# Performance work log

Measured on AMD Instinct MI355X. Metric: run time of the kernel, lower is better.

Reference implementation:

```python
import jax, jax.numpy as jnp
import numpy as np

N_POINTS = 131072
N_SEG = 16
C = 256
BN_EPS = 1e-5


def setup_inputs() -> dict:
    key = jax.random.key(0)
    ks = jax.random.split(key, 6)
    x = jax.random.normal(ks[0], (N_POINTS, C), jnp.float32)
    # Ragged segment end-offsets (cumulative counts), strictly increasing, last == N_POINTS.
    rng = np.random.default_rng(0)
    base = N_POINTS // N_SEG
    counts = base + rng.integers(-base // 32, base // 32, N_SEG)
    counts[-1] += N_POINTS - counts.sum()
    o = jnp.asarray(np.cumsum(counts), jnp.int32)
    s1 = 1.0 / np.sqrt(2 * C)  # linear1: Linear(2C -> C)
    s2 = 1.0 / np.sqrt(C)      # linear2: Linear(C -> C)
    W1 = jax.random.uniform(ks[1], (2 * C, C), jnp.float32, -s1, s1)
    b1 = jax.random.uniform(ks[2], (C,), jnp.float32, -s1, s1)
    W2 = jax.random.uniform(ks[3], (C, C), jnp.float32, -s2, s2)
    b2 = jax.random.uniform(ks[4], (C,), jnp.float32, -s2, s2)
    gamma = jnp.ones((C,), jnp.float32)
    beta = jnp.zeros((C,), jnp.float32)
    return {"x": x, "o": o, "W1": W1, "b1": b1, "W2": W2, "b2": b2,
            "gamma": gamma, "beta": beta}


def reference(x, o, W1, b1, W2, b2, gamma, beta):
    n, c = x.shape
    s = o.shape[0]
    # segment id per point from cumulative end-offsets
    seg_id = jnp.searchsorted(o, jnp.arange(n), side="right")  # [N]
    counts = jnp.concatenate([o[:1], o[1:] - o[:-1]])          # [S]
    # per-segment mean pooling (x_b.sum(0, True) / cnt)
    sums = jax.ops.segment_sum(x, seg_id, num_segments=s)      # [S, C]
    means = sums / counts[:, None].astype(x.dtype)
    # linear2: Linear(C, C) + ReLU on segment means
    y = jax.nn.relu(means @ W2 + b2)                           # [S, C]
    # broadcast-concat back to points, then linear1: Linear(2C, C)
    h = jnp.concatenate([x, y[seg_id]], axis=1) @ W1 + b1      # [N, C]
    # BatchNorm1d (training mode: batch statistics, biased variance) + ReLU
    mu = h.mean(axis=0)
    var = h.var(axis=0)
    out = jax.nn.relu((h - mu) * (gamma / jnp.sqrt(var + BN_EPS)) + beta)
    return out
```

## Files before the change

kernel.cpp:

```cpp
#include <hip/hip_runtime.h>
#include <stdint.h>

#define N_PTS 131072
#define NC 256
#define NSEG 16
#define BN_EPSF 1e-5f

typedef __attribute__((ext_vector_type(8))) short bf16x8;
typedef __attribute__((ext_vector_type(4))) float f32x4;

__device__ __forceinline__ unsigned short f2bf(float f) {
  union { float f; uint32_t u; } v; v.f = f;
  uint32_t u = v.u;
  uint32_t r = (u + 0x7fffu + ((u >> 16) & 1u)) >> 16;
  return (unsigned short)r;
}
__device__ __forceinline__ float bf2f(unsigned short h) {
  union { uint32_t u; float f; } v; v.u = ((uint32_t)h) << 16; return v.f;
}

__device__ __forceinline__ void bar_lds() {
  asm volatile("s_waitcnt lgkmcnt(0)" ::: "memory");
  __builtin_amdgcn_s_barrier();
}

__device__ __forceinline__ int swz(int col, int row) {
  return (col & ~63) | ((((col >> 3) & 7) ^ (row & 7)) << 3) | (col & 7);
}

__global__ __launch_bounds__(256) void k_prep(const float* __restrict__ W1,
                                              unsigned short* __restrict__ w1t,
                                              float* __restrict__ zerobuf) {
  int b = blockIdx.x, t = threadIdx.x;
  if (b >= 16) {
    int i = (b - 16) * 256 + t;
    if (i < 8448) zerobuf[i] = 0.f;
    return;
  }
  __shared__ float tile[64][65];
  int bx = b & 3, by = b >> 2;
  int k0 = by * 64, j0 = bx * 64;
  int r = t >> 6, c = t & 63;
#pragma unroll
  for (int i = 0; i < 16; ++i) {
    int kk = r + i * 4;
    tile[kk][c] = W1[(size_t)(k0 + kk) * NC + j0 + c];
  }
  __syncthreads();
#pragma unroll
  for (int i = 0; i < 16; ++i) {
    int jj = r + i * 4;
    w1t[(size_t)(j0 + jj) * NC + k0 + c] = f2bf(tile[c][jj]);
  }
}

__global__ __launch_bounds__(512, 2) void k_gemm1(
    const float* __restrict__ x, const int* __restrict__ o,
    const unsigned short* __restrict__ w1t,
    unsigned short* __restrict__ g_bf,
    float* __restrict__ seg_sums, float* __restrict__ hseg,
    float* __restrict__ gsumsq) {
  __shared__ __align__(16) unsigned short lA[2][64 * NC];
  __shared__ float s_xacc[2][NC];
  __shared__ float s_gA[NC], s_gB[NC], s_gq[NC];
  __shared__ int o_s[NSEG];
  int t = threadIdx.x, lane = t & 63, w = t >> 6;
  int rowB = blockIdx.x * 256;
  if (t < NSEG) o_s[t] = o[t];
  if (t < NC) { s_xacc[0][t] = 0.f; s_xacc[1][t] = 0.f; }
  __syncthreads();
  int sA = 0;
  while (o_s[sA] <= rowB) ++sA;
  int e = o_s[sA];
  int sB = (sA < NSEG - 1) ? sA + 1 : sA;

  bf16x8 Bf[4][2][2];
  {
    int jr0 = w * 32 + (lane & 15);
    int sl0 = lane >> 4;
#pragma unroll
    for (int kt = 0; kt < 4; ++kt)
#pragma unroll
      for (int kk = 0; kk < 2; ++kk)
#pragma unroll
        for (int nn = 0; nn < 2; ++nn)
          Bf[kt][kk][nn] = *(const bf16x8*)(
              w1t + (size_t)(jr0 + nn * 16) * NC + kt * 64 + (kk * 4 + sl0) * 8);
  }

  float4 xaccT = {0.f, 0.f, 0.f, 0.f}, xaccA = {0.f, 0.f, 0.f, 0.f};
  f32x4 pT[2] = {}, pA[2] = {}, pq[2] = {};
  f32x4 acc[4][2] = {};
  const float4* xv = (const float4*)x;
  int c0 = lane * 4;
  float4 xr[8];
#pragma unroll
  for (int i = 0; i < 8; ++i)
    xr[i] = xv[(size_t)(rowB + w + i * 8) * 64 + lane];

  for (int tile = 0; tile < 4; ++tile) {
    int row0 = rowB + tile * 64;
    int buf = tile & 1;
#pragma unroll
    for (int i = 0; i < 8; ++i) {
      int rl = w + i * 8;
      int r = row0 + rl;
      float4 v = xr[i];
      ushort4 b;
      b.x = f2bf(v.x); b.y = f2bf(v.y); b.z = f2bf(v.z); b.w = f2bf(v.w);
      *(ushort4*)(&lA[buf][rl * NC + swz(c0, rl)]) = b;
      xaccT.x += v.x; xaccT.y += v.y; xaccT.z += v.z; xaccT.w += v.w;
      bool inA = (r < e);
      xaccA.x += inA ? v.x : 0.f;
      xaccA.y += inA ? v.y : 0.f;
      xaccA.z += inA ? v.z : 0.f;
      xaccA.w += inA ? v.w : 0.f;
    }
    if (tile < 3) {
#pragma unroll
      for (int i = 0; i < 8; ++i)
        xr[i] = xv[(size_t)(row0 + 64 + w + i * 8) * 64 + lane];
    }
    bar_lds();

#pragma unroll
    for (int kt = 0; kt < 4; ++kt)
#pragma unroll
      for (int kk = 0; kk < 2; ++kk) {
        bf16x8 af[4];
        int sl = kk * 4 + (lane >> 4);
#pragma unroll
        for (int mm = 0; mm < 4; ++mm) {
          int r = mm * 16 + (lane & 15);
          af[mm] = *(const bf16x8*)(&lA[buf][r * NC + kt * 64 + ((sl ^ (r & 7)) << 3)]);
        }
#pragma unroll
        for (int mm = 0; mm < 4; ++mm)
#pragma unroll
          for (int nn = 0; nn < 2; ++nn)
            acc[mm][nn] = __builtin_amdgcn_mfma_f32_16x16x32_bf16(
                Bf[kt][kk][nn], af[mm], acc[mm][nn], 0, 0, 0);
      }

    int rl = lane & 15, q = lane >> 4;
#pragma unroll
    for (int mm = 0; mm < 4; ++mm) {
      int row = row0 + mm * 16 + rl;
      bool inA = (row < e);
#pragma unroll
      for (int nn = 0; nn < 2; ++nn) {
        f32x4 g = acc[mm][nn];
        ushort4 b;
        b.x = f2bf(g[0]); b.y = f2bf(g[1]); b.z = f2bf(g[2]); b.w = f2bf(g[3]);
        *(ushort4*)(g_bf + (size_t)row * NC + w * 32 + nn * 16 + q * 4) = b;
        pT[nn] += g;
        if (inA) pA[nn] += g;
        pq[nn] += g * g;
        acc[mm][nn] = (f32x4){0.f, 0.f, 0.f, 0.f};
      }
    }
  }

  atomicAdd(&s_xacc[0][c0 + 0], xaccA.x);
  atomicAdd(&s_xacc[0][c0 + 1], xaccA.y);
  atomicAdd(&s_xacc[0][c0 + 2], xaccA.z);
  atomicAdd(&s_xacc[0][c0 + 3], xaccA.w);
  atomicAdd(&s_xacc[1][c0 + 0], xaccT.x - xaccA.x);
  atomicAdd(&s_xacc[1][c0 + 1], xaccT.y - xaccA.y);
  atomicAdd(&s_xacc[1][c0 + 2], xaccT.z - xaccA.z);
  atomicAdd(&s_xacc[1][c0 + 3], xaccT.w - xaccA.w);
#pragma unroll
  for (int nn = 0; nn < 2; ++nn)
#pragma unroll
    for (int j = 0; j < 4; ++j) {
      float a = pA[nn][j], bb = pT[nn][j] - pA[nn][j], qq = pq[nn][j];
      a += __shfl_xor(a, 1, 64); a += __shfl_xor(a, 2, 64);
      a += __shfl_xor(a, 4, 64); a += __shfl_xor(a, 8, 64);
      bb += __shfl_xor(bb, 1, 64); bb += __shfl_xor(bb, 2, 64);
      bb += __shfl_xor(bb, 4, 64); bb += __shfl_xor(bb, 8, 64);
      qq += __shfl_xor(qq, 1, 64); qq += __shfl_xor(qq, 2, 64);
      qq += __shfl_xor(qq, 4, 64); qq += __shfl_xor(qq, 8, 64);
      pA[nn][j] = a; pT[nn][j] = bb; pq[nn][j] = qq;
    }
  if ((lane & 15) == 0) {
    int q = lane >> 4;
#pragma unroll
    for (int nn = 0; nn < 2; ++nn) {
      int cb = w * 32 + nn * 16 + q * 4;
#pragma unroll
      for (int j = 0; j < 4; ++j) {
        s_gA[cb + j] = pA[nn][j];
        s_gB[cb + j] = pT[nn][j];
        s_gq[cb + j] = pq[nn][j];
      }
    }
  }
  __syncthreads();
  if (t < NC) {
    atomicAdd(&seg_sums[sA * NC + t], s_xacc[0][t]);
    atomicAdd(&seg_sums[sB * NC + t], s_xacc[1][t]);
    atomicAdd(&hseg[sA * NC + t], s_gA[t]);
    atomicAdd(&hseg[sB * NC + t], s_gB[t]);
    atomicAdd(&gsumsq[t], s_gq[t]);
  }
}

__global__ __launch_bounds__(256) void k_seg_mlp(
    const int* __restrict__ o, const float* __restrict__ seg_sums,
    const float* __restrict__ W1, const float* __restrict__ b1,
    const float* __restrict__ W2, const float* __restrict__ b2,
    float* __restrict__ z) {
  __shared__ float mean_s[NC];
  __shared__ float y_s[NC];
  int b = blockIdx.x, j = threadIdx.x;
  int start = (b == 0) ? 0 : o[b - 1];
  float inv = 1.f / (float)(o[b] - start);
  mean_s[j] = seg_sums[b * NC + j] * inv;
  __syncthreads();
  float a = b2[j];
  for (int k = 0; k < NC; ++k) a += mean_s[k] * W2[k * NC + j];
  y_s[j] = fmaxf(a, 0.f);
  __syncthreads();
  float a2 = b1[j];
  for (int k = 0; k < NC; ++k) a2 += y_s[k] * W1[(NC + k) * NC + j];
  z[b * NC + j] = a2;
}

__global__ __launch_bounds__(256) void k_apply(
    const unsigned short* __restrict__ g_bf, const int* __restrict__ o,
    const float* __restrict__ z, const float* __restrict__ hseg,
    const float* __restrict__ gsumsq, const float* __restrict__ gamma,
    const float* __restrict__ beta, float* __restrict__ out) {
  __shared__ float s_scale[NC], s_shift[NC];
  __shared__ int o_s[NSEG];
  int t = threadIdx.x;
  int row0 = blockIdx.x * 64;
  if (t < NSEG) o_s[t] = o[t];
  __syncthreads();
  {
    float cs = 0.f, cq = gsumsq[t];
    int prev = 0;
#pragma unroll
    for (int s = 0; s < NSEG; ++s) {
      float cnt = (float)(o_s[s] - prev);
      prev = o_s[s];
      float hs = hseg[s * NC + t], zz = z[s * NC + t];
      cs += hs + cnt * zz;
      cq += (2.f * hs + cnt * zz) * zz;
    }
    float invN = 1.f / (float)N_PTS;
    float mu = cs * invN;
    float var = cq * invN - mu * mu;
    float sc = gamma[t] * rsqrtf(var + BN_EPSF);
    s_scale[t] = sc;
    s_shift[t] = beta[t] - mu * sc;
  }
  __syncthreads();
  int s0 = 0;
  while (o_s[s0] <= row0) ++s0;
  int e0 = o_s[s0];
  int s1 = (s0 < NSEG - 1) ? s0 + 1 : s0;
  int cg = (t & 31) * 8, rsub = t >> 5;
  float4 sc0 = *(const float4*)(s_scale + cg), sc1 = *(const float4*)(s_scale + cg + 4);
  float4 sh0 = *(const float4*)(s_shift + cg), sh1 = *(const float4*)(s_shift + cg + 4);
  float4 zA0 = *(const float4*)(z + s0 * NC + cg), zA1 = *(const float4*)(z + s0 * NC + cg + 4);
  float4 zB0 = *(const float4*)(z + s1 * NC + cg), zB1 = *(const float4*)(z + s1 * NC + cg + 4);
#pragma unroll
  for (int i = 0; i < 8; ++i) {
    int row = row0 + rsub + i * 8;
    uint4 hv = *(const uint4*)(g_bf + (size_t)row * NC + cg);
    bool inA = (row < e0);
    float4 z0 = inA ? zA0 : zB0;
    float4 z1 = inA ? zA1 : zB1;
    float4 o0, o1;
    o0.x = fmaxf((bf2f((unsigned short)(hv.x & 0xffffu)) + z0.x) * sc0.x + sh0.x, 0.f);
    o0.y = fmaxf((bf2f((unsigned short)(hv.x >> 16)) + z0.y) * sc0.y + sh0.y, 0.f);
    o0.z = fmaxf((bf2f((unsigned short)(hv.y & 0xffffu)) + z0.z) * sc0.z + sh0.z, 0.f);
    o0.w = fmaxf((bf2f((unsigned short)(hv.y >> 16)) + z0.w) * sc0.w + sh0.w, 0.f);
    o1.x = fmaxf((bf2f((unsigned short)(hv.z & 0xffffu)) + z1.x) * sc1.x + sh1.x, 0.f);
    o1.y = fmaxf((bf2f((unsigned short)(hv.z >> 16)) + z1.y) * sc1.y + sh1.y, 0.f);
    o1.z = fmaxf((bf2f((unsigned short)(hv.w & 0xffffu)) + z1.z) * sc1.z + sh1.z, 0.f);
    o1.w = fmaxf((bf2f((unsigned short)(hv.w >> 16)) + z1.w) * sc1.w + sh1.w, 0.f);
    *(float4*)(out + (size_t)row * NC + cg) = o0;
    *(float4*)(out + (size_t)row * NC + cg + 4) = o1;
  }
}

extern "C" void kernel_launch(void* const* d_in, const int* in_sizes, int n_in,
                              void* d_out, int out_size, void* d_ws, size_t ws_size,
                              hipStream_t stream) {
  const float* x = (const float*)d_in[0];
  const int* o = (const int*)d_in[1];
  const float* W1 = (const float*)d_in[2];
  const float* b1 = (const float*)d_in[3];
  const float* W2 = (const float*)d_in[4];
  const float* b2 = (const float*)d_in[5];
  const float* gamma = (const float*)d_in[6];
  const float* beta = (const float*)d_in[7];
  float* out = (float*)d_out;

  char* ws = (char*)d_ws;
  unsigned short* g_bf = (unsigned short*)ws;
  char* base2 = ws + 67108864;
  float* seg_sums = (float*)(base2);
  float* hseg     = (float*)(base2 + 16384);
  float* gsumsq   = (float*)(base2 + 32768);
  float* z        = (float*)(base2 + 33792);
  unsigned short* w1t = (unsigned short*)(base2 + 50176);

  k_prep<<<49, 256, 0, stream>>>(W1, w1t, seg_sums);
  k_gemm1<<<512, 512, 0, stream>>>(x, o, w1t, g_bf, seg_sums, hseg, gsumsq);
  k_seg_mlp<<<16, 256, 0, stream>>>(o, seg_sums, W1, b1, W2, b2, z);
  k_apply<<<2048, 256, 0, stream>>>(g_bf, o, z, hseg, gsumsq, gamma, beta, out);
}
```

Before: 313.5 us.

## Derive segment h-sums from segment x-sums and widen GEMM blocks to 1024 threads

The per-segment sums of the GEMM output (hseg) are no longer accumulated row by row in the GEMM epilogue. They are now computed once per segment in k_seg_mlp as seg_sums times the top half of W1, relying on linearity. In exchange the GEMM kernel runs 1024-thread blocks of 16 waves, each wave owning 16 output columns over 512 rows, which shrinks register state and the epilogue reductions. The risk is that each wave now re-reads the whole A tile from LDS for half as many MFMAs, which raises LDS traffic. hseg also shifts slightly in value because it is now computed from fp32 x against bf16 weights rather than from bf16 x.

```diff
diff --git a/kernel.cpp b/kernel.cpp
--- a/kernel.cpp
+++ b/kernel.cpp
@@ -54,18 +54,17 @@
   }
 }
 
-__global__ __launch_bounds__(512, 2) void k_gemm1(
+__global__ __launch_bounds__(1024, 4) void k_gemm1(
     const float* __restrict__ x, const int* __restrict__ o,
     const unsigned short* __restrict__ w1t,
     unsigned short* __restrict__ g_bf,
-    float* __restrict__ seg_sums, float* __restrict__ hseg,
-    float* __restrict__ gsumsq) {
+    float* __restrict__ seg_sums, float* __restrict__ gsumsq) {
   __shared__ __align__(16) unsigned short lA[2][64 * NC];
   __shared__ float s_xacc[2][NC];
-  __shared__ float s_gA[NC], s_gB[NC], s_gq[NC];
+  __shared__ float s_q[NC];
   __shared__ int o_s[NSEG];
   int t = threadIdx.x, lane = t & 63, w = t >> 6;
-  int rowB = blockIdx.x * 256;
+  int rowB = blockIdx.x * 512;
   if (t < NSEG) o_s[t] = o[t];
   if (t < NC) { s_xacc[0][t] = 0.f; s_xacc[1][t] = 0.f; }
   __syncthreads();
@@ -74,36 +73,34 @@
   int e = o_s[sA];
   int sB = (sA < NSEG - 1) ? sA + 1 : sA;
 
-  bf16x8 Bf[4][2][2];
+  bf16x8 Bf[4][2];
   {
-    int jr0 = w * 32 + (lane & 15);
+    int jr0 = w * 16 + (lane & 15);
     int sl0 = lane >> 4;
 #pragma unroll
     for (int kt = 0; kt < 4; ++kt)
 #pragma unroll
       for (int kk = 0; kk < 2; ++kk)
-#pragma unroll
-        for (int nn = 0; nn < 2; ++nn)
-          Bf[kt][kk][nn] = *(const bf16x8*)(
-              w1t + (size_t)(jr0 + nn * 16) * NC + kt * 64 + (kk * 4 + sl0) * 8);
+        Bf[kt][kk] = *(const bf16x8*)(
+            w1t + (size_t)jr0 * NC + kt * 64 + (kk * 4 + sl0) * 8);
   }
 
   float4 xaccT = {0.f, 0.f, 0.f, 0.f}, xaccA = {0.f, 0.f, 0.f, 0.f};
-  f32x4 pT[2] = {}, pA[2] = {}, pq[2] = {};
-  f32x4 acc[4][2] = {};
+  f32x4 pq = {};
+  f32x4 acc[4] = {};
   const float4* xv = (const float4*)x;
   int c0 = lane * 4;
-  float4 xr[8];
-#pragma unroll
-  for (int i = 0; i < 8; ++i)
-    xr[i] = xv[(size_t)(rowB + w + i * 8) * 64 + lane];
-
-  for (int tile = 0; tile < 4; ++tile) {
+  float4 xr[4];
+#pragma unroll
+  for (int i = 0; i < 4; ++i)
+    xr[i] = xv[(size_t)(rowB + w + i * 16) * 64 + lane];
+
+  for (int tile = 0; tile < 8; ++tile) {
     int row0 = rowB + tile * 64;
     int buf = tile & 1;
 #pragma unroll
-    for (int i = 0; i < 8; ++i) {
-      int rl = w + i * 8;
+    for (int i = 0; i < 4; ++i) {
+      int rl = w + i * 16;
       int r = row0 + rl;
       float4 v = xr[i];
       ushort4 b;
@@ -116,10 +113,10 @@
       xaccA.z += inA ? v.z : 0.f;
       xaccA.w += inA ? v.w : 0.f;
     }
-    if (tile < 3) {
-#pragma unroll
-      for (int i = 0; i < 8; ++i)
-        xr[i] = xv[(size_t)(row0 + 64 + w + i * 8) * 64 + lane];
+    if (tile < 7) {
+#pragma unroll
+      for (int i = 0; i < 4; ++i)
+        xr[i] = xv[(size_t)(row0 + 64 + w + i * 16) * 64 + lane];
     }
     bar_lds();
 
@@ -136,28 +133,20 @@
         }
 #pragma unroll
         for (int mm = 0; mm < 4; ++mm)
-#pragma unroll
-          for (int nn = 0; nn < 2; ++nn)
-            acc[mm][nn] = __builtin_amdgcn_mfma_f32_16x16x32_bf16(
-                Bf[kt][kk][nn], af[mm], acc[mm][nn], 0, 0, 0);
+          acc[mm] = __builtin_amdgcn_mfma_f32_16x16x32_bf16(
+              Bf[kt][kk], af[mm], acc[mm], 0, 0, 0);
       }
 
     int rl = lane & 15, q = lane >> 4;
 #pragma unroll
     for (int mm = 0; mm < 4; ++mm) {
       int row = row0 + mm * 16 + rl;
-      bool inA = (row < e);
-#pragma unroll
-      for (int nn = 0; nn < 2; ++nn) {
-        f32x4 g = acc[mm][nn];
-        ushort4 b;
-        b.x = f2bf(g[0]); b.y = f2bf(g[1]); b.z = f2bf(g[2]); b.w = f2bf(g[3]);
-        *(ushort4*)(g_bf + (size_t)row * NC + w * 32 + nn * 16 + q * 4) = b;
-        pT[nn] += g;
-        if (inA) pA[nn] += g;
-        pq[nn] += g * g;
-        acc[mm][nn] = (f32x4){0.f, 0.f, 0.f, 0.f};
-      }
+      f32x4 g = acc[mm];
+      ushort4 b;
+      b.x = f2bf(g[0]); b.y = f2bf(g[1]); b.z = f2bf(g[2]); b.w = f2bf(g[3]);
+      *(ushort4*)(g_bf + (size_t)row * NC + w * 16 + q * 4) = b;
+      pq += g * g;
+      acc[mm] = (f32x4){0.f, 0.f, 0.f, 0.f};
     }
   }
 
@@ -170,38 +159,22 @@
   atomicAdd(&s_xacc[1][c0 + 2], xaccT.z - xaccA.z);
   atomicAdd(&s_xacc[1][c0 + 3], xaccT.w - xaccA.w);
 #pragma unroll
-  for (int nn = 0; nn < 2; ++nn)
-#pragma unroll
-    for (int j = 0; j < 4; ++j) {
-      float a = pA[nn][j], bb = pT[nn][j] - pA[nn][j], qq = pq[nn][j];
-      a += __shfl_xor(a, 1, 64); a += __shfl_xor(a, 2, 64);
-      a += __shfl_xor(a, 4, 64); a += __shfl_xor(a, 8, 64);
-      bb += __shfl_xor(bb, 1, 64); bb += __shfl_xor(bb, 2, 64);
-      bb += __shfl_xor(bb, 4, 64); bb += __shfl_xor(bb, 8, 64);
-      qq += __shfl_xor(qq, 1, 64); qq += __shfl_xor(qq, 2, 64);
-      qq += __shfl_xor(qq, 4, 64); qq += __shfl_xor(qq, 8, 64);
-      pA[nn][j] = a; pT[nn][j] = bb; pq[nn][j] = qq;
-    }
+  for (int j = 0; j < 4; ++j) {
+    float qq = pq[j];
+    qq += __shfl_xor(qq, 1, 64); qq += __shfl_xor(qq, 2, 64);
+    qq += __shfl_xor(qq, 4, 64); qq += __shfl_xor(qq, 8, 64);
+    pq[j] = qq;
+  }
   if ((lane & 15) == 0) {
     int q = lane >> 4;
 #pragma unroll
-    for (int nn = 0; nn < 2; ++nn) {
-      int cb = w * 32 + nn * 16 + q * 4;
-#pragma unroll
-      for (int j = 0; j < 4; ++j) {
-        s_gA[cb + j] = pA[nn][j];
-        s_gB[cb + j] = pT[nn][j];
-        s_gq[cb + j] = pq[nn][j];
-      }
-    }
+    for (int j = 0; j < 4; ++j) s_q[w * 16 + q * 4 + j] = pq[j];
   }
   __syncthreads();
   if (t < NC) {
     atomicAdd(&seg_sums[sA * NC + t], s_xacc[0][t]);
     atomicAdd(&seg_sums[sB * NC + t], s_xacc[1][t]);
-    atomicAdd(&hseg[sA * NC + t], s_gA[t]);
-    atomicAdd(&hseg[sB * NC + t], s_gB[t]);
-    atomicAdd(&gsumsq[t], s_gq[t]);
+    atomicAdd(&gsumsq[t], s_q[t]);
   }
 }
 
@@ -209,14 +182,21 @@
     const int* __restrict__ o, const float* __restrict__ seg_sums,
     const float* __restrict__ W1, const float* __restrict__ b1,
     const float* __restrict__ W2, const float* __restrict__ b2,
-    float* __restrict__ z) {
+    const unsigned short* __restrict__ w1t,
+    float* __restrict__ z, float* __restrict__ hseg) {
+  __shared__ float ss_s[NC];
   __shared__ float mean_s[NC];
   __shared__ float y_s[NC];
   int b = blockIdx.x, j = threadIdx.x;
   int start = (b == 0) ? 0 : o[b - 1];
   float inv = 1.f / (float)(o[b] - start);
-  mean_s[j] = seg_sums[b * NC + j] * inv;
-  __syncthreads();
+  float ssv = seg_sums[b * NC + j];
+  ss_s[j] = ssv;
+  mean_s[j] = ssv * inv;
+  __syncthreads();
+  float hs = 0.f;
+  for (int k = 0; k < NC; ++k) hs += ss_s[k] * bf2f(w1t[(size_t)j * NC + k]);
+  hseg[b * NC + j] = hs;
   float a = b2[j];
   for (int k = 0; k < NC; ++k) a += mean_s[k] * W2[k * NC + j];
   y_s[j] = fmaxf(a, 0.f);
@@ -309,7 +289,7 @@
   unsigned short* w1t = (unsigned short*)(base2 + 50176);
 
   k_prep<<<49, 256, 0, stream>>>(W1, w1t, seg_sums);
-  k_gemm1<<<512, 512, 0, stream>>>(x, o, w1t, g_bf, seg_sums, hseg, gsumsq);
-  k_seg_mlp<<<16, 256, 0, stream>>>(o, seg_sums, W1, b1, W2, b2, z);
+  k_gemm1<<<256, 1024, 0, stream>>>(x, o, w1t, g_bf, seg_sums, gsumsq);
+  k_seg_mlp<<<16, 256, 0, stream>>>(o, seg_sums, W1, b1, W2, b2, w1t, z, hseg);
   k_apply<<<2048, 256, 0, stream>>>(g_bf, o, z, hseg, gsumsq, gamma, beta, out);
 }
```

Result: no change. 317.2 us (+1.2%).
